# Optimization experiments

Hardware: AMD Instinct MI355X
Metric: run time of the kernel (lower is better)

## Reference

```python
import jax, jax.numpy as jnp
import numpy as np

N_USERS, N_ITEMS, N_RATINGS = 10000, 10000, 5
D = 64
KU, KS, KB = 50, 50, 50
BATCH = 2048


def setup_inputs() -> dict:
    key = jax.random.key(0)
    ks = iter(jax.random.split(key, 64))

    def nrm(shape, scale=0.05):
        return jax.random.normal(next(ks), shape, dtype=jnp.float32) * scale

    def rint(shape, hi):
        return jax.random.randint(next(ks), shape, 0, hi, dtype=jnp.int32)

    inp = {
        'user_idx': rint((BATCH,), N_USERS),
        'item_idx': rint((BATCH,), N_ITEMS),
        'C': rint((N_USERS, KU), N_ITEMS),
        'N': rint((N_USERS, KS), N_USERS),
        'B': rint((N_ITEMS, KB), N_USERS),
        'R': rint((N_USERS, N_ITEMS), N_RATINGS),
        'user_emb': nrm((N_USERS, D)),
        'item_emb': nrm((N_ITEMS, D)),
        'opinion_emb': nrm((N_RATINGS, D)),
    }
    for pre in ('ia', 'ua'):
        inp[pre + '_Wg'] = nrm((2 * D, D)); inp[pre + '_bg'] = nrm((D,))
    for pre in ('ia', 'sa', 'ua'):
        inp[pre + '_Wa1'] = nrm((2 * D, D)); inp[pre + '_ba1'] = nrm((D,))
        inp[pre + '_Wa2'] = nrm((D, 1));     inp[pre + '_ba2'] = nrm((1,))
        inp[pre + '_W'] = nrm((D, D));       inp[pre + '_b'] = nrm((D,))
    for pre in ('fu', 'rp'):
        inp[pre + '_W1'] = nrm((2 * D, D)); inp[pre + '_b1'] = nrm((D,))
        inp[pre + '_W2'] = nrm((D, D));     inp[pre + '_b2'] = nrm((D,))
    inp['fu_W3'] = nrm((D, D)); inp['fu_b3'] = nrm((D,))
    inp['rp_W3'] = nrm((D, 1)); inp['rp_b3'] = nrm((1,))
    return inp


def _att(x, ctx, Wa1, ba1, Wa2, ba2):
    # x: [n,K,D] neighbor features, ctx: [n,D] query embedding
    cat = jnp.concatenate([x, jnp.broadcast_to(ctx[:, None, :], x.shape)], axis=-1)
    h = jax.nn.relu(cat @ Wa1 + ba1)
    return jax.nn.softmax((h @ Wa2 + ba2)[..., 0], axis=-1)  # [n,K]


def _agg(x, ctx, Wa1, ba1, Wa2, ba2, W, b):
    a = _att(x, ctx, Wa1, ba1, Wa2, ba2)
    return jax.nn.relu(jnp.einsum('nk,nkd->nd', a, x) @ W + b)


def _forward(user_idx, item_idx, C, N, B, R, user_emb, item_emb, opinion_emb,
             ia_Wg, ia_bg, ia_Wa1, ia_ba1, ia_Wa2, ia_ba2, ia_W, ia_b,
             sa_Wa1, sa_ba1, sa_Wa2, sa_ba2, sa_W, sa_b,
             ua_Wg, ua_bg, ua_Wa1, ua_ba1, ua_Wa2, ua_ba2, ua_W, ua_b,
             fu_W1, fu_b1, fu_W2, fu_b2, fu_W3, fu_b3,
             rp_W1, rp_b1, rp_W2, rp_b2, rp_W3, rp_b3):
    def item_space_agg(u_ids):
        Cn = C[u_ids]                                  # [n,KU] item neighbors
        r = R[u_ids[:, None], Cn]                      # [n,KU] rating indices
        x = jax.nn.relu(jnp.concatenate([item_emb[Cn], opinion_emb[r]], axis=-1) @ ia_Wg + ia_bg)
        return _agg(x, user_emb[u_ids], ia_Wa1, ia_ba1, ia_Wa2, ia_ba2, ia_W, ia_b)

    h_I_batch = item_space_agg(user_idx)
    h_I_all = item_space_agg(jnp.arange(user_emb.shape[0]))
    # social aggregation over h_I of social neighbors
    h_nbr = h_I_all[N[user_idx]]                       # [B,KS,D]
    h_S = _agg(h_nbr, user_emb[user_idx], sa_Wa1, sa_ba1, sa_Wa2, sa_ba2, sa_W, sa_b)
    # user factor fusion MLP (num_hidden_layers=3)
    h = jnp.concatenate([h_I_batch, h_S], axis=-1)
    h = jax.nn.relu(h @ fu_W1 + fu_b1)
    h = jax.nn.relu(h @ fu_W2 + fu_b2)
    h = jax.nn.relu(h @ fu_W3 + fu_b3)
    # item modeling: aggregate users who rated item j
    Bn = B[item_idx]                                   # [B,KB]
    r = R[Bn, item_idx[:, None]]                       # [B,KB]
    f = jax.nn.relu(jnp.concatenate([user_emb[Bn], opinion_emb[r]], axis=-1) @ ua_Wg + ua_bg)
    z = _agg(f, item_emb[item_idx], ua_Wa1, ua_ba1, ua_Wa2, ua_ba2, ua_W, ua_b)
    # rating prediction MLP
    g = jnp.concatenate([h, z], axis=-1)
    g = jax.nn.relu(g @ rp_W1 + rp_b1)
    g = jax.nn.relu(g @ rp_W2 + rp_b2)
    return (g @ rp_W3 + rp_b3)[:, 0]                   # [batch]


def reference(user_idx, item_idx, C, N, B, R, user_emb, item_emb, opinion_emb,
              ia_Wg, ia_bg, ia_Wa1, ia_ba1, ia_Wa2, ia_ba2, ia_W, ia_b,
              sa_Wa1, sa_ba1, sa_Wa2, sa_ba2, sa_W, sa_b,
              ua_Wg, ua_bg, ua_Wa1, ua_ba1, ua_Wa2, ua_ba2, ua_W, ua_b,
              fu_W1, fu_b1, fu_W2, fu_b2, fu_W3, fu_b3,
              rp_W1, rp_b1, rp_W2, rp_b2, rp_W3, rp_b3):
    return _forward(user_idx, item_idx, C, N, B, R, user_emb, item_emb, opinion_emb,
                    ia_Wg, ia_bg, ia_Wa1, ia_ba1, ia_Wa2, ia_ba2, ia_W, ia_b,
                    sa_Wa1, sa_ba1, sa_Wa2, sa_ba2, sa_W, sa_b,
                    ua_Wg, ua_bg, ua_Wa1, ua_ba1, ua_Wa2, ua_ba2, ua_W, ua_b,
                    fu_W1, fu_b1, fu_W2, fu_b2, fu_W3, fu_b3,
                    rp_W1, rp_b1, rp_W2, rp_b2, rp_W3, rp_b3)
```

## Files before the change

### kernel.cpp

```cpp
#include <hip/hip_runtime.h>
#include <hip/hip_fp16.h>

#define D 64
#define KP 50
#define NIT 10000

#define RFL __builtin_amdgcn_readfirstlane

typedef _Float16 half8 __attribute__((ext_vector_type(8)));
typedef float floatx4 __attribute__((ext_vector_type(4)));

__device__ inline float rlanef(float v, int l) {
  return __int_as_float(__builtin_amdgcn_readlane(__float_as_int(v), l));
}

__device__ inline half8 loadA_f32(const float* __restrict__ src, int kc,
                                  int lane) {
  const float* p = src + (size_t)(lane & 15) * D + kc * 32 + 8 * (lane >> 4);
  float4 lo = *(const float4*)p;
  float4 hi = *(const float4*)(p + 4);
  half8 a;
  a[0] = (_Float16)lo.x; a[1] = (_Float16)lo.y;
  a[2] = (_Float16)lo.z; a[3] = (_Float16)lo.w;
  a[4] = (_Float16)hi.x; a[5] = (_Float16)hi.y;
  a[6] = (_Float16)hi.z; a[7] = (_Float16)hi.w;
  return a;
}

__device__ inline half8 loadB_f32(const float* __restrict__ W, int kc, int t,
                                  int lane) {
  const float* p =
      W + (size_t)(kc * 32 + 8 * (lane >> 4)) * D + 16 * t + (lane & 15);
  half8 b;
#pragma unroll
  for (int j = 0; j < 8; ++j) b[j] = (_Float16)p[(size_t)j * D];
  return b;
}


__device__ inline float score_row_h(const __half* __restrict__ xa,
                                    const float* __restrict__ ia,
                                    const float* __restrict__ w2) {
  float p0 = 0.f, p1 = 0.f;
#pragma unroll
  for (int j = 0; j < D; j += 8) {
    float4 q = *(const float4*)&xa[j];
    const __half2* h2 = (const __half2*)&q;
#pragma unroll
    for (int m = 0; m < 4; ++m) {
      float2 f = __half22float2(h2[m]);
      p0 = fmaf(fmaxf(f.x + ia[j + 2 * m + 0], 0.f), w2[j + 2 * m + 0], p0);
      p1 = fmaf(fmaxf(f.y + ia[j + 2 * m + 1], 0.f), w2[j + 2 * m + 1], p1);
    }
  }
  return p0 + p1;
}

__device__ inline float softmax50(float val, int lane) {
  val = (lane < KP) ? val : -1e30f;
  float m = val;
#pragma unroll
  for (int o = 1; o < 64; o <<= 1) m = fmaxf(m, __shfl_xor(m, o, 64));
  float e = (lane < KP) ? __expf(val - m) : 0.f;
  float s = e;
#pragma unroll
  for (int o = 1; o < 64; o <<= 1) s += __shfl_xor(s, o, 64);
  return e / s;
}

__device__ inline float wsum_rows_h(float a, int ix,
                                    const __half* __restrict__ T, int lane) {
  float v0 = 0.f, v1 = 0.f;
#pragma unroll 10
  for (int k = 0; k < KP; k += 2) {
    const int i0 = __builtin_amdgcn_readlane(ix, k);
    const int i1 = __builtin_amdgcn_readlane(ix, k + 1);
    const float a0 = rlanef(a, k);
    const float a1 = rlanef(a, k + 1);
    v0 = fmaf(a0, (float)T[(size_t)i0 * 128 + 64 + lane], v0);
    v1 = fmaf(a1, (float)T[(size_t)i1 * 128 + 64 + lane], v1);
  }
  return v0 + v1;
}

template <bool RELU>
__device__ inline float mv64b(float vin, const float* __restrict__ W,
                              const float* __restrict__ bias, int lane) {
  float acc = bias[lane];
#pragma unroll 8
  for (int j = 0; j < D; ++j)
    acc = fmaf(rlanef(vin, j), W[j * D + lane], acc);
  return RELU ? fmaxf(acc, 0.f) : acc;
}

__device__ inline float mv128b(float lo, float hi, const float* __restrict__ W,
                               const float* __restrict__ bias, int lane) {
  float acc = bias[lane];
#pragma unroll 8
  for (int j = 0; j < D; ++j)
    acc = fmaf(rlanef(lo, j), W[j * D + lane], acc);
#pragma unroll 8
  for (int j = 0; j < D; ++j)
    acc = fmaf(rlanef(hi, j), W[(D + j) * D + lane], acc);
  return fmaxf(acc, 0.f);
}

#define LSTR 72

__global__ __launch_bounds__(64) void k_tabs(
    const float* __restrict__ item_emb, const float* __restrict__ user_emb,
    const float* __restrict__ op_emb, const float* __restrict__ ia_Wg,
    const float* __restrict__ ia_bg, const float* __restrict__ ua_Wg,
    const float* __restrict__ ua_bg, const float* __restrict__ ia_Wa1,
    const float* __restrict__ ia_ba1, const float* __restrict__ sa_Wa1,
    const float* __restrict__ sa_ba1, const float* __restrict__ ua_Wa1,
    const float* __restrict__ ua_ba1, __half* __restrict__ XXA5,
    __half* __restrict__ FFA5, float* __restrict__ IAu,
    float* __restrict__ SAu, float* __restrict__ UAt, int NU_) {
  __shared__ _Float16 ldsX[16 * LSTR];
  __shared__ _Float16 ldsA[16 * LSTR];
  const int lane = threadIdx.x;
  const int nbl = NU_ >> 4;
  const int s = blockIdx.x / nbl, blk = blockIdx.x % nbl;
  const int g0 = blk * 16;
  const int q = lane >> 4, p = lane & 15;

  if (s >= 2) {
    const float* src = (s == 4) ? item_emb : user_emb;
    const float* W = (s == 2)   ? ia_Wa1 + D * D
                     : (s == 3) ? sa_Wa1 + D * D
                                : ua_Wa1 + D * D;
    const float* bias = (s == 2) ? ia_ba1 : (s == 3) ? sa_ba1 : ua_ba1;
    float* dst = (s == 2) ? IAu : (s == 3) ? SAu : UAt;
    half8 a0 = loadA_f32(src + (size_t)g0 * D, 0, lane);
    half8 a1 = loadA_f32(src + (size_t)g0 * D, 1, lane);
#pragma unroll
    for (int t = 0; t < 4; ++t) {
      floatx4 acc = {0.f, 0.f, 0.f, 0.f};
      half8 b0 = loadB_f32(W, 0, t, lane);
      half8 b1 = loadB_f32(W, 1, t, lane);
      acc = __builtin_amdgcn_mfma_f32_16x16x32_f16(a0, b0, acc, 0, 0, 0);
      acc = __builtin_amdgcn_mfma_f32_16x16x32_f16(a1, b1, acc, 0, 0, 0);
      const float bv = bias[16 * t + p];
#pragma unroll
      for (int i = 0; i < 4; ++i)
        dst[(size_t)(g0 + 4 * q + i) * D + 16 * t + p] = acc[i] + bv;
    }
    return;
  }

  const float* emb = s ? user_emb : item_emb;
  const float* Wg = s ? ua_Wg : ia_Wg;
  const float* bg = s ? ua_bg : ia_bg;
  const float* Wa = s ? ua_Wa1 : ia_Wa1;
  __half* dst = s ? FFA5 : XXA5;

  float opbg[5];
#pragma unroll
  for (int r = 0; r < 5; ++r) opbg[r] = bg[lane];
  for (int j = 0; j < D; ++j) {
    const float w = Wg[(size_t)(D + j) * D + lane];
#pragma unroll
    for (int r = 0; r < 5; ++r) opbg[r] = fmaf(op_emb[r * D + j], w, opbg[r]);
  }

  half8 a0 = loadA_f32(emb + (size_t)g0 * D, 0, lane);
  half8 a1 = loadA_f32(emb + (size_t)g0 * D, 1, lane);
  floatx4 base[4];
  half8 wa[4][2];
#pragma unroll
  for (int t = 0; t < 4; ++t) {
    base[t] = {0.f, 0.f, 0.f, 0.f};
    half8 b0 = loadB_f32(Wg, 0, t, lane);
    half8 b1 = loadB_f32(Wg, 1, t, lane);
    base[t] = __builtin_amdgcn_mfma_f32_16x16x32_f16(a0, b0, base[t], 0, 0, 0);
    base[t] = __builtin_amdgcn_mfma_f32_16x16x32_f16(a1, b1, base[t], 0, 0, 0);
    wa[t][0] = loadB_f32(Wa, 0, t, lane);
    wa[t][1] = loadB_f32(Wa, 1, t, lane);
  }

  for (int r = 0; r < 5; ++r) {
#pragma unroll
    for (int t = 0; t < 4; ++t) {
      const float ob = __shfl(opbg[r], p + 16 * t, 64);
#pragma unroll
      for (int i = 0; i < 4; ++i)
        ldsX[(4 * q + i) * LSTR + 16 * t + p] =
            (_Float16)fmaxf(base[t][i] + ob, 0.f);
    }
    half8 xa0 = *(const half8*)&ldsX[p * LSTR + 0 * 32 + 8 * q];
    half8 xa1 = *(const half8*)&ldsX[p * LSTR + 1 * 32 + 8 * q];
    floatx4 acc[4];
#pragma unroll
    for (int t = 0; t < 4; ++t) {
      acc[t] = {0.f, 0.f, 0.f, 0.f};
      acc[t] =
          __builtin_amdgcn_mfma_f32_16x16x32_f16(xa0, wa[t][0], acc[t], 0, 0, 0);
      acc[t] =
          __builtin_amdgcn_mfma_f32_16x16x32_f16(xa1, wa[t][1], acc[t], 0, 0, 0);
    }
#pragma unroll
    for (int t = 0; t < 4; ++t)
#pragma unroll
      for (int i = 0; i < 4; ++i)
        ldsA[(4 * q + i) * LSTR + 16 * t + p] = (_Float16)acc[t][i];
    const uint32_t* srcbuf =
        (lane < 32) ? (const uint32_t*)ldsA : (const uint32_t*)ldsX;
    const int dl = lane & 31;
    for (int m = 0; m < 16; ++m) {
      const uint32_t val = srcbuf[m * (LSTR / 2) + dl];
      uint32_t* rowp = (uint32_t*)(dst + ((size_t)(g0 + m) * 5 + r) * 128);
      rowp[lane] = val;
    }
  }
}

__global__ __launch_bounds__(256, 8) void k_hIall(
    const int* __restrict__ C, const int* __restrict__ Rm,
    const __half* __restrict__ XXA5, const float* __restrict__ IAu,
    const float* __restrict__ ia_Wa2, const float* __restrict__ ia_W,
    const float* __restrict__ ia_b, const float* __restrict__ sa_Wa1,
    __half* __restrict__ HHA) {
  const int lane = threadIdx.x & 63;
  const int u = RFL(blockIdx.x * 4 + (threadIdx.x >> 6));
  const int kk = lane < KP ? lane : KP - 1;
  const int c = C[u * KP + kk];
  const int ix = c * 5 + Rm[(size_t)u * NIT + c];
  float sc = score_row_h(XXA5 + (size_t)ix * 128, IAu + (size_t)u * D, ia_Wa2);
  float a = softmax50(sc, lane);
  float v = wsum_rows_h(a, ix, XXA5, lane);
  float h = mv64b<true>(v, ia_W, ia_b, lane);
  float ha = 0.f;
#pragma unroll 8
  for (int j = 0; j < D; ++j)
    ha = fmaf(rlanef(h, j), sa_Wa1[j * D + lane], ha);
  HHA[(size_t)u * 128 + lane] = __float2half(ha);
  HHA[(size_t)u * 128 + 64 + lane] = __float2half(h);
}

__global__ __launch_bounds__(256, 8) void k_batch(
    const int* __restrict__ user_idx, const int* __restrict__ item_idx,
    const int* __restrict__ Nn, const int* __restrict__ Bm,
    const int* __restrict__ Rm, const __half* __restrict__ HHA,
    const __half* __restrict__ FFA5, const float* __restrict__ SAu,
    const float* __restrict__ UAt, const float* __restrict__ sa_Wa2,
    const float* __restrict__ sa_W, const float* __restrict__ sa_b,
    const float* __restrict__ ua_Wa2, const float* __restrict__ ua_W,
    const float* __restrict__ ua_b, const float* __restrict__ fu_W1,
    const float* __restrict__ fu_b1, const float* __restrict__ fu_W2,
    const float* __restrict__ fu_b2, const float* __restrict__ fu_W3,
    const float* __restrict__ fu_b3, const float* __restrict__ rp_W1,
    const float* __restrict__ rp_b1, const float* __restrict__ rp_W2,
    const float* __restrict__ rp_b2, const float* __restrict__ rp_W3,
    const float* __restrict__ rp_b3, float* __restrict__ out) {
  const int lane = threadIdx.x & 63;
  const int b = RFL(blockIdx.x * 4 + (threadIdx.x >> 6));
  const int u = RFL(user_idx[b]);
  const int it = RFL(item_idx[b]);
  const int kk = lane < KP ? lane : KP - 1;
  const int nix = Nn[u * KP + kk];
  const int bn = Bm[it * KP + kk];
  const int ix2 = bn * 5 + Rm[(size_t)bn * NIT + it];
  const float hIu = (float)HHA[(size_t)u * 128 + 64 + lane];
  float sc = score_row_h(HHA + (size_t)nix * 128, SAu + (size_t)u * D, sa_Wa2);
  float a = softmax50(sc, lane);
  float v = wsum_rows_h(a, nix, HHA, lane);
  float hS = mv64b<true>(v, sa_W, sa_b, lane);
  float sc2 =
      score_row_h(FFA5 + (size_t)ix2 * 128, UAt + (size_t)it * D, ua_Wa2);
  float a2 = softmax50(sc2, lane);
  float v2 = wsum_rows_h(a2, ix2, FFA5, lane);
  float z = mv64b<true>(v2, ua_W, ua_b, lane);
  float h = mv128b(hIu, hS, fu_W1, fu_b1, lane);
  h = mv64b<true>(h, fu_W2, fu_b2, lane);
  h = mv64b<true>(h, fu_W3, fu_b3, lane);
  float g = mv128b(h, z, rp_W1, rp_b1, lane);
  g = mv64b<true>(g, rp_W2, rp_b2, lane);
  float pp = g * rp_W3[lane];
#pragma unroll
  for (int o = 1; o < 64; o <<= 1) pp += __shfl_xor(pp, o, 64);
  if (lane == 0) out[b] = pp + rp_b3[0];
}

extern "C" void kernel_launch(void* const* d_in, const int* in_sizes, int n_in,
                              void* d_out, int out_size, void* d_ws,
                              size_t ws_size, hipStream_t stream) {
  const int* user_idx = (const int*)d_in[0];
  const int* item_idx = (const int*)d_in[1];
  const int* C = (const int*)d_in[2];
  const int* Nn = (const int*)d_in[3];
  const int* Bm = (const int*)d_in[4];
  const int* Rm = (const int*)d_in[5];
  const float* user_emb = (const float*)d_in[6];
  const float* item_emb = (const float*)d_in[7];
  const float* opinion_emb = (const float*)d_in[8];
  const float* ia_Wg = (const float*)d_in[9];
  const float* ia_bg = (const float*)d_in[10];
  const float* ua_Wg = (const float*)d_in[11];
  const float* ua_bg = (const float*)d_in[12];
  const float* ia_Wa1 = (const float*)d_in[13];
  const float* ia_ba1 = (const float*)d_in[14];
  const float* ia_Wa2 = (const float*)d_in[15];
  const float* ia_W = (const float*)d_in[17];
  const float* ia_b = (const float*)d_in[18];
  const float* sa_Wa1 = (const float*)d_in[19];
  const float* sa_ba1 = (const float*)d_in[20];
  const float* sa_Wa2 = (const float*)d_in[21];
  const float* sa_W = (const float*)d_in[23];
  const float* sa_b = (const float*)d_in[24];
  const float* ua_Wa1 = (const float*)d_in[25];
  const float* ua_ba1 = (const float*)d_in[26];
  const float* ua_Wa2 = (const float*)d_in[27];
  const float* ua_W = (const float*)d_in[29];
  const float* ua_b = (const float*)d_in[30];
  const float* fu_W1 = (const float*)d_in[31];
  const float* fu_b1 = (const float*)d_in[32];
  const float* fu_W2 = (const float*)d_in[33];
  const float* fu_b2 = (const float*)d_in[34];
  const float* rp_W1 = (const float*)d_in[35];
  const float* rp_b1 = (const float*)d_in[36];
  const float* rp_W2 = (const float*)d_in[37];
  const float* rp_b2 = (const float*)d_in[38];
  const float* fu_W3 = (const float*)d_in[39];
  const float* fu_b3 = (const float*)d_in[40];
  const float* rp_W3 = (const float*)d_in[41];
  const float* rp_b3 = (const float*)d_in[42];

  const int NU = in_sizes[6] / D;
  const int B = in_sizes[0];

  __half* XXA5 = (__half*)d_ws;
  __half* FFA5 = XXA5 + (size_t)NU * 5 * 128;
  __half* HHA = FFA5 + (size_t)NU * 5 * 128;
  float* IAu = (float*)(HHA + (size_t)NU * 128);
  float* SAu = IAu + (size_t)NU * D;
  float* UAt = SAu + (size_t)NU * D;

  const int nbl = NU / 16;

  k_tabs<<<5 * nbl, 64, 0, stream>>>(item_emb, user_emb, opinion_emb, ia_Wg,
                                     ia_bg, ua_Wg, ua_bg, ia_Wa1, ia_ba1,
                                     sa_Wa1, sa_ba1, ua_Wa1, ua_ba1, XXA5,
                                     FFA5, IAu, SAu, UAt, NU);
  k_hIall<<<NU / 4, 256, 0, stream>>>(C, Rm, XXA5, IAu, ia_Wa2, ia_W, ia_b,
                                      sa_Wa1, HHA);
  k_batch<<<B / 4, 256, 0, stream>>>(user_idx, item_idx, Nn, Bm, Rm, HHA, FFA5,
                                     SAu, UAt, sa_Wa2, sa_W, sa_b, ua_Wa2,
                                     ua_W, ua_b, fu_W1, fu_b1, fu_W2, fu_b2,
                                     fu_W3, fu_b3, rp_W1, rp_b1, rp_W2, rp_b2,
                                     rp_W3, rp_b3, (float*)d_out);
}
```

Baseline: 88.67 us.

## Split per-row MLPs into separate MFMA kernels with split-fp16 precision

The dense per-row matrix-vector chains (readlane-broadcast FMAs) in the aggregation kernels move into new kernels that batch 16 rows per wavefront and run them as 16x16x32 MFMA GEMMs. fp32 accuracy is kept by splitting operands into hi/lo fp16 parts. The gather/softmax/weighted-sum stages now write intermediate vectors to workspace and stop. This removes the serial scalar MLP work but adds two kernel launches, extra global round trips for the intermediates, three MFMAs per product, and several barriers.

```diff
diff --git a/kernel.cpp b/kernel.cpp
--- a/kernel.cpp
+++ b/kernel.cpp
@@ -37,6 +37,74 @@
   return b;
 }
 
+struct AB { half8 hi, lo; };
+
+__device__ inline AB splitA(const float* src, int stride, int kc, int lane) {
+  const float* p =
+      src + (size_t)(lane & 15) * stride + kc * 32 + 8 * (lane >> 4);
+  AB r;
+#pragma unroll
+  for (int j = 0; j < 8; ++j) {
+    float x = p[j];
+    _Float16 h = (_Float16)x;
+    r.hi[j] = h;
+    r.lo[j] = (_Float16)(x - (float)h);
+  }
+  return r;
+}
+
+__device__ inline AB splitB(const float* __restrict__ W, int kc, int t,
+                            int lane) {
+  const float* p =
+      W + (size_t)(kc * 32 + 8 * (lane >> 4)) * D + 16 * t + (lane & 15);
+  AB r;
+#pragma unroll
+  for (int j = 0; j < 8; ++j) {
+    float x = p[(size_t)j * D];
+    _Float16 h = (_Float16)x;
+    r.hi[j] = h;
+    r.lo[j] = (_Float16)(x - (float)h);
+  }
+  return r;
+}
+
+__device__ inline floatx4 mfma3(AB a, AB b, floatx4 acc) {
+  acc = __builtin_amdgcn_mfma_f32_16x16x32_f16(a.hi, b.hi, acc, 0, 0, 0);
+  acc = __builtin_amdgcn_mfma_f32_16x16x32_f16(a.hi, b.lo, acc, 0, 0, 0);
+  acc = __builtin_amdgcn_mfma_f32_16x16x32_f16(a.lo, b.hi, acc, 0, 0, 0);
+  return acc;
+}
+
+__device__ inline void gemm64(const float* Asrc, int As,
+                              const float* __restrict__ W, int lane,
+                              floatx4 acc[4]) {
+  AB a0 = splitA(Asrc, As, 0, lane);
+  AB a1 = splitA(Asrc, As, 1, lane);
+#pragma unroll
+  for (int t = 0; t < 4; ++t) {
+    floatx4 z = {0.f, 0.f, 0.f, 0.f};
+    AB b0 = splitB(W, 0, t, lane);
+    AB b1 = splitB(W, 1, t, lane);
+    z = mfma3(a0, b0, z);
+    z = mfma3(a1, b1, z);
+    acc[t] = z;
+  }
+}
+
+__device__ inline void cstore(const floatx4 acc[4],
+                              const float* __restrict__ bias, bool relu,
+                              float* Lb, int S, int lane) {
+  const int q = lane >> 4, p = lane & 15;
+#pragma unroll
+  for (int t = 0; t < 4; ++t) {
+    const float bv = bias ? bias[16 * t + p] : 0.f;
+#pragma unroll
+    for (int i = 0; i < 4; ++i) {
+      float v = acc[t][i] + bv;
+      Lb[(4 * q + i) * S + 16 * t + p] = relu ? fmaxf(v, 0.f) : v;
+    }
+  }
+}
 
 __device__ inline float score_row_h(const __half* __restrict__ xa,
                                     const float* __restrict__ ia,
@@ -81,28 +149,6 @@
     v1 = fmaf(a1, (float)T[(size_t)i1 * 128 + 64 + lane], v1);
   }
   return v0 + v1;
-}
-
-template <bool RELU>
-__device__ inline float mv64b(float vin, const float* __restrict__ W,
-                              const float* __restrict__ bias, int lane) {
-  float acc = bias[lane];
-#pragma unroll 8
-  for (int j = 0; j < D; ++j)
-    acc = fmaf(rlanef(vin, j), W[j * D + lane], acc);
-  return RELU ? fmaxf(acc, 0.f) : acc;
-}
-
-__device__ inline float mv128b(float lo, float hi, const float* __restrict__ W,
-                               const float* __restrict__ bias, int lane) {
-  float acc = bias[lane];
-#pragma unroll 8
-  for (int j = 0; j < D; ++j)
-    acc = fmaf(rlanef(lo, j), W[j * D + lane], acc);
-#pragma unroll 8
-  for (int j = 0; j < D; ++j)
-    acc = fmaf(rlanef(hi, j), W[(D + j) * D + lane], acc);
-  return fmaxf(acc, 0.f);
 }
 
 #define LSTR 72
@@ -180,6 +226,7 @@
   }
 
   for (int r = 0; r < 5; ++r) {
+    __syncthreads();
 #pragma unroll
     for (int t = 0; t < 4; ++t) {
       const float ob = __shfl(opbg[r], p + 16 * t, 64);
@@ -188,22 +235,24 @@
         ldsX[(4 * q + i) * LSTR + 16 * t + p] =
             (_Float16)fmaxf(base[t][i] + ob, 0.f);
     }
+    __syncthreads();
     half8 xa0 = *(const half8*)&ldsX[p * LSTR + 0 * 32 + 8 * q];
     half8 xa1 = *(const half8*)&ldsX[p * LSTR + 1 * 32 + 8 * q];
     floatx4 acc[4];
 #pragma unroll
     for (int t = 0; t < 4; ++t) {
       acc[t] = {0.f, 0.f, 0.f, 0.f};
-      acc[t] =
-          __builtin_amdgcn_mfma_f32_16x16x32_f16(xa0, wa[t][0], acc[t], 0, 0, 0);
-      acc[t] =
-          __builtin_amdgcn_mfma_f32_16x16x32_f16(xa1, wa[t][1], acc[t], 0, 0, 0);
+      acc[t] = __builtin_amdgcn_mfma_f32_16x16x32_f16(xa0, wa[t][0], acc[t], 0,
+                                                      0, 0);
+      acc[t] = __builtin_amdgcn_mfma_f32_16x16x32_f16(xa1, wa[t][1], acc[t], 0,
+                                                      0, 0);
     }
 #pragma unroll
     for (int t = 0; t < 4; ++t)
 #pragma unroll
       for (int i = 0; i < 4; ++i)
         ldsA[(4 * q + i) * LSTR + 16 * t + p] = (_Float16)acc[t][i];
+    __syncthreads();
     const uint32_t* srcbuf =
         (lane < 32) ? (const uint32_t*)ldsA : (const uint32_t*)ldsX;
     const int dl = lane & 31;
@@ -215,12 +264,10 @@
   }
 }
 
-__global__ __launch_bounds__(256, 8) void k_hIall(
+__global__ __launch_bounds__(256, 8) void k_hv(
     const int* __restrict__ C, const int* __restrict__ Rm,
     const __half* __restrict__ XXA5, const float* __restrict__ IAu,
-    const float* __restrict__ ia_Wa2, const float* __restrict__ ia_W,
-    const float* __restrict__ ia_b, const float* __restrict__ sa_Wa1,
-    __half* __restrict__ HHA) {
+    const float* __restrict__ ia_Wa2, float* __restrict__ Vh) {
   const int lane = threadIdx.x & 63;
   const int u = RFL(blockIdx.x * 4 + (threadIdx.x >> 6));
   const int kk = lane < KP ? lane : KP - 1;
@@ -228,31 +275,51 @@
   const int ix = c * 5 + Rm[(size_t)u * NIT + c];
   float sc = score_row_h(XXA5 + (size_t)ix * 128, IAu + (size_t)u * D, ia_Wa2);
   float a = softmax50(sc, lane);
-  float v = wsum_rows_h(a, ix, XXA5, lane);
-  float h = mv64b<true>(v, ia_W, ia_b, lane);
-  float ha = 0.f;
-#pragma unroll 8
-  for (int j = 0; j < D; ++j)
-    ha = fmaf(rlanef(h, j), sa_Wa1[j * D + lane], ha);
-  HHA[(size_t)u * 128 + lane] = __float2half(ha);
-  HHA[(size_t)u * 128 + 64 + lane] = __float2half(h);
-}
-
-__global__ __launch_bounds__(256, 8) void k_batch(
+  Vh[(size_t)u * D + lane] = wsum_rows_h(a, ix, XXA5, lane);
+}
+
+__global__ __launch_bounds__(64) void k_hmlp(const float* __restrict__ Vh,
+                                             const float* __restrict__ ia_W,
+                                             const float* __restrict__ ia_b,
+                                             const float* __restrict__ sa_Wa1,
+                                             __half* __restrict__ HHA) {
+  __shared__ float Lh[16 * 68];
+  __shared__ _Float16 sA[16 * LSTR];
+  __shared__ _Float16 sB[16 * LSTR];
+  const int lane = threadIdx.x;
+  const int g0 = blockIdx.x * 16;
+  const int q = lane >> 4, p = lane & 15;
+  floatx4 acc[4];
+  gemm64(Vh + (size_t)g0 * D, D, ia_W, lane, acc);
+  cstore(acc, ia_b, true, Lh, 68, lane);
+  __syncthreads();
+  floatx4 acc2[4];
+  gemm64(Lh, 68, sa_Wa1, lane, acc2);
+#pragma unroll
+  for (int t = 0; t < 4; ++t)
+#pragma unroll
+    for (int i = 0; i < 4; ++i)
+      sA[(4 * q + i) * LSTR + 16 * t + p] = (_Float16)acc2[t][i];
+  for (int m = 0; m < 16; ++m)
+    sB[m * LSTR + lane] = (_Float16)Lh[m * 68 + lane];
+  __syncthreads();
+  const uint32_t* srcbuf =
+      (lane < 32) ? (const uint32_t*)sA : (const uint32_t*)sB;
+  const int dl = lane & 31;
+  for (int m = 0; m < 16; ++m) {
+    const uint32_t val = srcbuf[m * (LSTR / 2) + dl];
+    ((uint32_t*)(HHA + (size_t)(g0 + m) * 128))[lane] = val;
+  }
+}
+
+__global__ __launch_bounds__(256, 8) void k_bagg(
     const int* __restrict__ user_idx, const int* __restrict__ item_idx,
     const int* __restrict__ Nn, const int* __restrict__ Bm,
     const int* __restrict__ Rm, const __half* __restrict__ HHA,
     const __half* __restrict__ FFA5, const float* __restrict__ SAu,
     const float* __restrict__ UAt, const float* __restrict__ sa_Wa2,
-    const float* __restrict__ sa_W, const float* __restrict__ sa_b,
-    const float* __restrict__ ua_Wa2, const float* __restrict__ ua_W,
-    const float* __restrict__ ua_b, const float* __restrict__ fu_W1,
-    const float* __restrict__ fu_b1, const float* __restrict__ fu_W2,
-    const float* __restrict__ fu_b2, const float* __restrict__ fu_W3,
-    const float* __restrict__ fu_b3, const float* __restrict__ rp_W1,
-    const float* __restrict__ rp_b1, const float* __restrict__ rp_W2,
-    const float* __restrict__ rp_b2, const float* __restrict__ rp_W3,
-    const float* __restrict__ rp_b3, float* __restrict__ out) {
+    const float* __restrict__ ua_Wa2, float* __restrict__ VS,
+    float* __restrict__ VZ) {
   const int lane = threadIdx.x & 63;
   const int b = RFL(blockIdx.x * 4 + (threadIdx.x >> 6));
   const int u = RFL(user_idx[b]);
@@ -261,25 +328,105 @@
   const int nix = Nn[u * KP + kk];
   const int bn = Bm[it * KP + kk];
   const int ix2 = bn * 5 + Rm[(size_t)bn * NIT + it];
-  const float hIu = (float)HHA[(size_t)u * 128 + 64 + lane];
   float sc = score_row_h(HHA + (size_t)nix * 128, SAu + (size_t)u * D, sa_Wa2);
   float a = softmax50(sc, lane);
-  float v = wsum_rows_h(a, nix, HHA, lane);
-  float hS = mv64b<true>(v, sa_W, sa_b, lane);
+  VS[(size_t)b * D + lane] = wsum_rows_h(a, nix, HHA, lane);
   float sc2 =
       score_row_h(FFA5 + (size_t)ix2 * 128, UAt + (size_t)it * D, ua_Wa2);
   float a2 = softmax50(sc2, lane);
-  float v2 = wsum_rows_h(a2, ix2, FFA5, lane);
-  float z = mv64b<true>(v2, ua_W, ua_b, lane);
-  float h = mv128b(hIu, hS, fu_W1, fu_b1, lane);
-  h = mv64b<true>(h, fu_W2, fu_b2, lane);
-  h = mv64b<true>(h, fu_W3, fu_b3, lane);
-  float g = mv128b(h, z, rp_W1, rp_b1, lane);
-  g = mv64b<true>(g, rp_W2, rp_b2, lane);
-  float pp = g * rp_W3[lane];
-#pragma unroll
-  for (int o = 1; o < 64; o <<= 1) pp += __shfl_xor(pp, o, 64);
-  if (lane == 0) out[b] = pp + rp_b3[0];
+  VZ[(size_t)b * D + lane] = wsum_rows_h(a2, ix2, FFA5, lane);
+}
+
+__global__ __launch_bounds__(64) void k_bmlp(
+    const int* __restrict__ user_idx, const float* __restrict__ VS,
+    const float* __restrict__ VZ, const __half* __restrict__ HHA,
+    const float* __restrict__ sa_W, const float* __restrict__ sa_b,
+    const float* __restrict__ ua_W, const float* __restrict__ ua_b,
+    const float* __restrict__ fu_W1, const float* __restrict__ fu_b1,
+    const float* __restrict__ fu_W2, const float* __restrict__ fu_b2,
+    const float* __restrict__ fu_W3, const float* __restrict__ fu_b3,
+    const float* __restrict__ rp_W1, const float* __restrict__ rp_b1,
+    const float* __restrict__ rp_W2, const float* __restrict__ rp_b2,
+    const float* __restrict__ rp_W3, const float* __restrict__ rp_b3,
+    float* __restrict__ out) {
+  __shared__ float L1[16 * 68];
+  __shared__ float L2[16 * 68];
+  __shared__ float L3[16 * 68];
+  const int lane = threadIdx.x;
+  const int r0 = blockIdx.x * 16;
+  const int q = lane >> 4, p = lane & 15;
+  floatx4 acc[4];
+  gemm64(VS + (size_t)r0 * D, D, sa_W, lane, acc);
+  cstore(acc, sa_b, true, L1, 68, lane);
+  gemm64(VZ + (size_t)r0 * D, D, ua_W, lane, acc);
+  cstore(acc, ua_b, true, L2, 68, lane);
+  __syncthreads();
+  const int um = user_idx[r0 + p];
+  half8 hA0 = *(const half8*)(HHA + (size_t)um * 128 + 64 + 0 * 32 + 8 * q);
+  half8 hA1 = *(const half8*)(HHA + (size_t)um * 128 + 64 + 1 * 32 + 8 * q);
+  {
+    AB a2 = splitA(L1, 68, 0, lane);
+    AB a3 = splitA(L1, 68, 1, lane);
+#pragma unroll
+    for (int t = 0; t < 4; ++t) {
+      floatx4 z = {0.f, 0.f, 0.f, 0.f};
+      AB b0 = splitB(fu_W1, 0, t, lane);
+      AB b1 = splitB(fu_W1, 1, t, lane);
+      z = __builtin_amdgcn_mfma_f32_16x16x32_f16(hA0, b0.hi, z, 0, 0, 0);
+      z = __builtin_amdgcn_mfma_f32_16x16x32_f16(hA0, b0.lo, z, 0, 0, 0);
+      z = __builtin_amdgcn_mfma_f32_16x16x32_f16(hA1, b1.hi, z, 0, 0, 0);
+      z = __builtin_amdgcn_mfma_f32_16x16x32_f16(hA1, b1.lo, z, 0, 0, 0);
+      AB b2 = splitB(fu_W1 + 64 * D, 0, t, lane);
+      AB b3 = splitB(fu_W1 + 64 * D, 1, t, lane);
+      z = mfma3(a2, b2, z);
+      z = mfma3(a3, b3, z);
+      acc[t] = z;
+    }
+    __syncthreads();
+    cstore(acc, fu_b1, true, L3, 68, lane);
+  }
+  __syncthreads();
+  gemm64(L3, 68, fu_W2, lane, acc);
+  __syncthreads();
+  cstore(acc, fu_b2, true, L1, 68, lane);
+  __syncthreads();
+  gemm64(L1, 68, fu_W3, lane, acc);
+  __syncthreads();
+  cstore(acc, fu_b3, true, L3, 68, lane);
+  __syncthreads();
+  {
+    AB a0 = splitA(L3, 68, 0, lane);
+    AB a1 = splitA(L3, 68, 1, lane);
+    AB a2 = splitA(L2, 68, 0, lane);
+    AB a3 = splitA(L2, 68, 1, lane);
+#pragma unroll
+    for (int t = 0; t < 4; ++t) {
+      floatx4 z = {0.f, 0.f, 0.f, 0.f};
+      AB b0 = splitB(rp_W1, 0, t, lane);
+      AB b1 = splitB(rp_W1, 1, t, lane);
+      AB b2 = splitB(rp_W1 + 64 * D, 0, t, lane);
+      AB b3 = splitB(rp_W1 + 64 * D, 1, t, lane);
+      z = mfma3(a0, b0, z);
+      z = mfma3(a1, b1, z);
+      z = mfma3(a2, b2, z);
+      z = mfma3(a3, b3, z);
+      acc[t] = z;
+    }
+    __syncthreads();
+    cstore(acc, rp_b1, true, L1, 68, lane);
+  }
+  __syncthreads();
+  gemm64(L1, 68, rp_W2, lane, acc);
+  __syncthreads();
+  cstore(acc, rp_b2, true, L3, 68, lane);
+  __syncthreads();
+  float pp = 0.f;
+#pragma unroll
+  for (int j = 0; j < 16; ++j)
+    pp = fmaf(L3[p * 68 + 16 * q + j], rp_W3[16 * q + j], pp);
+  pp += __shfl_xor(pp, 16, 64);
+  pp += __shfl_xor(pp, 32, 64);
+  if (lane < 16) out[r0 + lane] = pp + rp_b3[0];
 }
 
 extern "C" void kernel_launch(void* const* d_in, const int* in_sizes, int n_in,
@@ -335,6 +482,9 @@
   float* IAu = (float*)(HHA + (size_t)NU * 128);
   float* SAu = IAu + (size_t)NU * D;
   float* UAt = SAu + (size_t)NU * D;
+  float* Vh = UAt + (size_t)NU * D;
+  float* VS = Vh + (size_t)NU * D;
+  float* VZ = VS + (size_t)B * D;
 
   const int nbl = NU / 16;
 
@@ -342,11 +492,12 @@
                                      ia_bg, ua_Wg, ua_bg, ia_Wa1, ia_ba1,
                                      sa_Wa1, sa_ba1, ua_Wa1, ua_ba1, XXA5,
                                      FFA5, IAu, SAu, UAt, NU);
-  k_hIall<<<NU / 4, 256, 0, stream>>>(C, Rm, XXA5, IAu, ia_Wa2, ia_W, ia_b,
-                                      sa_Wa1, HHA);
-  k_batch<<<B / 4, 256, 0, stream>>>(user_idx, item_idx, Nn, Bm, Rm, HHA, FFA5,
-                                     SAu, UAt, sa_Wa2, sa_W, sa_b, ua_Wa2,
-                                     ua_W, ua_b, fu_W1, fu_b1, fu_W2, fu_b2,
-                                     fu_W3, fu_b3, rp_W1, rp_b1, rp_W2, rp_b2,
-                                     rp_W3, rp_b3, (float*)d_out);
-}
+  k_hv<<<NU / 4, 256, 0, stream>>>(C, Rm, XXA5, IAu, ia_Wa2, Vh);
+  k_hmlp<<<nbl, 64, 0, stream>>>(Vh, ia_W, ia_b, sa_Wa1, HHA);
+  k_bagg<<<B / 4, 256, 0, stream>>>(user_idx, item_idx, Nn, Bm, Rm, HHA, FFA5,
+                                    SAu, UAt, sa_Wa2, ua_Wa2, VS, VZ);
+  k_bmlp<<<B / 16, 64, 0, stream>>>(user_idx, VS, VZ, HHA, sa_W, sa_b, ua_W,
+                                    ua_b, fu_W1, fu_b1, fu_W2, fu_b2, fu_W3,
+                                    fu_b3, rp_W1, rp_b1, rp_W2, rp_b2, rp_W3,
+                                    rp_b3, (float*)d_out);
+}
```

New measurement: 107.1 us. 20.8% more time.
